# Kernel tuning notes

Hardware: AMD Instinct MI355X
Metric: run time of the kernel (lower is better)

Reference implementation:

```python
import jax, jax.numpy as jnp
from jax import lax
import numpy as np

V, E, H, F = 50257, 256, 512, 2
B, T = 128, 1024


def setup_inputs() -> dict:
    key = jax.random.key(0)
    ks = jax.random.split(key, 12)
    # zero-padded token ids: nonzero ids up to a random length, then 0-padding
    tok = jax.random.randint(ks[0], (B, T), 1, V)
    lengths = jax.random.randint(ks[1], (B,), 2, T + 1)  # at least 2 real tokens
    pos = jnp.arange(T)[None, :]
    tokens = jnp.where(pos < lengths[:, None], tok, 0)
    s = 0.02
    return {
        "tokens": tokens,
        "emb": jax.random.normal(ks[2], (V, E), jnp.float32) * s,
        "W_ih": jax.random.normal(ks[3], (4 * H, E), jnp.float32) * s,
        "b_ih": jax.random.normal(ks[4], (4 * H,), jnp.float32) * s,
        "W_hh": jax.random.normal(ks[5], (4 * H, H), jnp.float32) * s,
        "b_hh": jax.random.normal(ks[6], (4 * H,), jnp.float32) * s,
        "W_proj": jax.random.normal(ks[7], (H, 2 * H), jnp.float32) * s,
        "b_proj": jax.random.normal(ks[8], (H,), jnp.float32) * s,
        "W_out": jax.random.normal(ks[9], (F, H), jnp.float32) * s,
        "b_out": jax.random.normal(ks[10], (F,), jnp.float32) * s,
        "h0": jax.random.normal(ks[11], (B, H), jnp.float32),
        "c0": jax.random.normal(jax.random.fold_in(key, 99), (B, H), jnp.float32),
    }


def reference(tokens, emb, W_ih, b_ih, W_hh, b_hh, W_proj, b_proj, W_out, b_out, h0, c0):
    Bsz, Tlen = tokens.shape
    # sent_len = (index of first zero) - 1 ; if no zero, len(sent) - 1
    is_zero = tokens == 0
    first_zero = jnp.where(jnp.any(is_zero, axis=1), jnp.argmax(is_zero, axis=1), Tlen)
    sent_len = first_zero - 1  # negative wraps like python list indexing

    x = emb[tokens]  # [B, T, E]

    def step(carry, xt):
        h, c = carry
        gates = xt @ W_ih.T + b_ih + h @ W_hh.T + b_hh  # [B, 4H]
        i, f, g, o = jnp.split(gates, 4, axis=1)
        i = jax.nn.sigmoid(i)
        f = jax.nn.sigmoid(f)
        g = jnp.tanh(g)
        o = jax.nn.sigmoid(o)
        c = f * c + i * g
        h = o * jnp.tanh(c)
        return (h, c), (h, c)

    _, (hs, cs) = lax.scan(step, (h0, c0), jnp.swapaxes(x, 0, 1))  # [T, B, H]
    bidx = jnp.arange(Bsz)
    last = jnp.concatenate([hs[sent_len, bidx], cs[sent_len, bidx]], axis=1)  # [B, 2H]
    y = last @ W_proj.T + b_proj
    return y @ W_out.T + b_out
```

## Files before the change

### kernel.cpp

```cpp
#include <hip/hip_runtime.h>
#include <math.h>

#define B 128
#define T 1024
#define E 256
#define H 512

#define HBUF_OFF   0
#define LASTH_OFF  (2*65536)
#define LASTC_OFF  (3*65536)
#define FLAG_OFF   (4*65536)

__device__ __forceinline__ float sigm_f(float x) {
    return 1.f / (1.f + expf(-x));
}
__device__ __forceinline__ float tanh_f(float x) {
    return tanhf(x);
}

__device__ __forceinline__ void reduce32(float (&v)[32], int lane) {
#define RR(MASK, HALF)                                                 \
    {                                                                  \
        const bool hi = (lane & MASK) != 0;                            \
        _Pragma("unroll")                                              \
        for (int i = 0; i < HALF; ++i) {                               \
            const float mine   = hi ? v[i + HALF] : v[i];              \
            const float theirs = hi ? v[i] : v[i + HALF];              \
            v[i] = mine + __shfl_xor(theirs, MASK);                    \
        }                                                              \
    }
    RR(32, 16)
    RR(16, 8)
    RR(8, 4)
    RR(4, 2)
    RR(2, 1)
#undef RR
    v[0] = v[0] + __shfl_xor(v[0], 1);
}

__global__ __launch_bounds__(1024, 4) void lstm_persistent(
    const int* __restrict__ tokens, const float* __restrict__ emb,
    const float* __restrict__ W_ih, const float* __restrict__ b_ih,
    const float* __restrict__ W_hh, const float* __restrict__ b_hh,
    const float* __restrict__ h0, const float* __restrict__ c0,
    float* __restrict__ ws) {
    const int tid = threadIdx.x, bid = blockIdx.x;
    const int g = bid >> 5, m = bid & 31;

    float* h_buf  = ws + HBUF_OFF;
    float* last_h = ws + LASTH_OFF;
    float* last_c = ws + LASTC_OFF;
    int*   flags  = (int*)(ws + FLAG_OFF) + g * 64;

    __shared__ __align__(16) float xh[16 * 772];
    __shared__ float sgate[4][16][17];
    __shared__ int   s_L[16];
    __shared__ float s_c[256];
    __shared__ int   s_go;
    __shared__ float lds_pad[8192];

    {
        volatile float* vp = lds_pad;
        for (int i = tid; i < 8192; i += 1024) vp[i] = 0.f;
    }
    if (tid == 0) s_go = 0;

    if (tid < 16) s_L[tid] = T;
    __syncthreads();
    {
        const int b = tid >> 6;
        const int* tb = tokens + (size_t)(g * 16 + b) * T;
        int fz = T;
        for (int p = (tid & 63); p < T; p += 64)
            if (tb[p] == 0) fz = min(fz, p);
        atomicMin(&s_L[b], fz);
    }
    __syncthreads();
    if (tid < 16) {
        const int f = s_L[tid];
        s_L[tid] = (f == 0 || f == T) ? T : f;
    }
    __syncthreads();
    int Tg = 0;
#pragma unroll
    for (int i = 0; i < 16; ++i) Tg = max(Tg, s_L[i]);

    if (tid < 256) {
        const int uli = tid >> 4, bi = tid & 15;
        s_c[tid] = c0[(size_t)(g * 16 + bi) * H + (m * 16 + uli)];
    }

    {
        const int b = tid >> 6, kq4 = tid & 63;
        const int tok = tokens[(size_t)(g * 16 + b) * T + 0];
        ((float4*)&xh[b * 772])[kq4] =
            ((const float4*)emb)[(size_t)tok * 64 + kq4];
    }

    const int lane = tid & 63;
    const int w    = tid >> 6;
    const int unit = m * 16 + w;
    const float4* Wi4 = (const float4*)W_ih;
    const float4* Wh4 = (const float4*)W_hh;
    float4 wx[4], wh0[4], wh1[4];
#pragma unroll
    for (int G = 0; G < 4; ++G) {
        wx[G]  = Wi4[((size_t)G * H + unit) * 64 + lane];
        wh0[G] = Wh4[((size_t)G * H + unit) * 128 + lane];
        wh1[G] = Wh4[((size_t)G * H + unit) * 128 + 64 + lane];
    }

    const int ul2 = tid >> 4, b2 = tid & 15;
    const int unit2 = m * 16 + (ul2 & 15);
    const int bg = g * 16 + b2;
    const float bi_i = b_ih[unit2],         bh_i = b_hh[unit2];
    const float bi_f = b_ih[H + unit2],     bh_f = b_hh[H + unit2];
    const float bi_g = b_ih[2 * H + unit2], bh_g = b_hh[2 * H + unit2];
    const float bi_o = b_ih[3 * H + unit2], bh_o = b_hh[3 * H + unit2];

    __syncthreads();

    float v[32];

    for (int t = 0; t < Tg; ++t) {
#pragma unroll
        for (int bb = 0; bb < 8; ++bb) {
            const float4 x = ((const float4*)&xh[bb * 772])[lane];
#pragma unroll
            for (int G = 0; G < 4; ++G) {
                float p = wx[G].x * x.x;
                p = fmaf(wx[G].y, x.y, p);
                p = fmaf(wx[G].z, x.z, p);
                p = fmaf(wx[G].w, x.w, p);
                v[G * 8 + bb] = p;
            }
        }

        if (t > 0) {
            if (tid < 64) {
                const int* slot = &flags[tid & 31];
                while (true) {
                    const int fv = __hip_atomic_load(slot, __ATOMIC_RELAXED,
                                                     __HIP_MEMORY_SCOPE_AGENT);
                    if (__all(fv >= t)) break;
                    __builtin_amdgcn_s_sleep(1);
                }
                if (tid == 0)
                    __hip_atomic_store(&s_go, t, __ATOMIC_RELAXED,
                                       __HIP_MEMORY_SCOPE_WORKGROUP);
            } else {
                while (__hip_atomic_load(&s_go, __ATOMIC_RELAXED,
                                         __HIP_MEMORY_SCOPE_WORKGROUP) < t)
                    __builtin_amdgcn_s_sleep(1);
            }
        }

        if (t == 0) {
            const int b = tid >> 6, l = tid & 63;
            const float4* h04 = (const float4*)(h0 + (size_t)(g * 16 + b) * H);
            float4* dst = (float4*)&xh[b * 772 + 256];
            dst[l]      = h04[l];
            dst[64 + l] = h04[64 + l];
        } else {
            const unsigned long long* hs8 = (const unsigned long long*)
                (h_buf + (size_t)(t & 1) * (H * B));
            float2 hv[4];
#pragma unroll
            for (int j = 0; j < 4; ++j) {
                const int idx = j * 1024 + tid;
                const int u = idx >> 3, bp = idx & 7;
                unsigned long long val = __hip_atomic_load(
                    &hs8[(size_t)u * 64 + g * 8 + bp],
                    __ATOMIC_RELAXED, __HIP_MEMORY_SCOPE_AGENT);
                hv[j] = __builtin_bit_cast(float2, val);
            }
#pragma unroll
            for (int j = 0; j < 4; ++j) {
                const int idx = j * 1024 + tid;
                const int u = idx >> 3, bp = idx & 7;
                xh[(2 * bp) * 772 + 256 + u]     = hv[j].x;
                xh[(2 * bp + 1) * 772 + 256 + u] = hv[j].y;
            }
        }
        __syncthreads();

#pragma unroll
        for (int bb = 0; bb < 8; ++bb) {
            const float4 ha = ((const float4*)&xh[bb * 772])[64 + lane];
            const float4 hb = ((const float4*)&xh[bb * 772])[128 + lane];
#pragma unroll
            for (int G = 0; G < 4; ++G) {
                float p = v[G * 8 + bb];
                p = fmaf(wh0[G].x, ha.x, p);
                p = fmaf(wh0[G].y, ha.y, p);
                p = fmaf(wh0[G].z, ha.z, p);
                p = fmaf(wh0[G].w, ha.w, p);
                p = fmaf(wh1[G].x, hb.x, p);
                p = fmaf(wh1[G].y, hb.y, p);
                p = fmaf(wh1[G].z, hb.z, p);
                p = fmaf(wh1[G].w, hb.w, p);
                v[G * 8 + bb] = p;
            }
        }
        reduce32(v, lane);
        if ((lane & 1) == 0) {
            const int vi = (lane >> 1) & 31;
            sgate[vi >> 3][w][vi & 7] = v[0];
        }

#pragma unroll
        for (int bb = 0; bb < 8; ++bb) {
            const float4 x  = ((const float4*)&xh[(8 + bb) * 772])[lane];
            const float4 ha = ((const float4*)&xh[(8 + bb) * 772])[64 + lane];
            const float4 hb = ((const float4*)&xh[(8 + bb) * 772])[128 + lane];
#pragma unroll
            for (int G = 0; G < 4; ++G) {
                float p = wx[G].x * x.x;
                p = fmaf(wx[G].y, x.y, p);
                p = fmaf(wx[G].z, x.z, p);
                p = fmaf(wx[G].w, x.w, p);
                p = fmaf(wh0[G].x, ha.x, p);
                p = fmaf(wh0[G].y, ha.y, p);
                p = fmaf(wh0[G].z, ha.z, p);
                p = fmaf(wh0[G].w, ha.w, p);
                p = fmaf(wh1[G].x, hb.x, p);
                p = fmaf(wh1[G].y, hb.y, p);
                p = fmaf(wh1[G].z, hb.z, p);
                p = fmaf(wh1[G].w, hb.w, p);
                v[G * 8 + bb] = p;
            }
        }
        reduce32(v, lane);
        if ((lane & 1) == 0) {
            const int vi = (lane >> 1) & 31;
            sgate[vi >> 3][w][8 + (vi & 7)] = v[0];
        }

        float4 xreg;
        const bool do_stage = (t + 1 < Tg);
        if (do_stage) {
            const int b = tid >> 6, kq4 = tid & 63;
            const int tok = tokens[(size_t)(g * 16 + b) * T + (t + 1)];
            xreg = ((const float4*)emb)[(size_t)tok * 64 + kq4];
        }
        __syncthreads();

        if (tid < 256) {
            const float ai = sgate[0][ul2][b2] + bi_i + bh_i;
            const float af = sgate[1][ul2][b2] + bi_f + bh_f;
            const float ag = sgate[2][ul2][b2] + bi_g + bh_g;
            const float ao = sgate[3][ul2][b2] + bi_o + bh_o;

            const float ig = sigm_f(ai);
            const float fg = sigm_f(af);
            const float gv = tanh_f(ag);
            const float og = sigm_f(ao);

            const float c_old = s_c[tid];
            const float c_new = fg * c_old + ig * gv;
            const float h_new = og * tanh_f(c_new);
            s_c[tid] = c_new;

            const int idx = unit2 * B + bg;
            __hip_atomic_store(&h_buf[(size_t)((t + 1) & 1) * (H * B) + idx],
                               h_new, __ATOMIC_RELAXED,
                               __HIP_MEMORY_SCOPE_AGENT);
            if (t == s_L[b2] - 1) {
                last_h[idx] = h_new;
                last_c[idx] = c_new;
            }
        }

        if (do_stage) {
            __syncthreads();
            if (tid == 0)
                __hip_atomic_store(&flags[m], t + 1, __ATOMIC_RELAXED,
                                   __HIP_MEMORY_SCOPE_AGENT);
            {
                const int b = tid >> 6, kq4 = tid & 63;
                ((float4*)&xh[b * 772])[kq4] = xreg;
            }
            __syncthreads();
        }
    }
}

__global__ __launch_bounds__(256) void final_kernel(
    const float* __restrict__ ws_ro, const float* __restrict__ W_proj,
    const float* __restrict__ b_proj, const float* __restrict__ W_out,
    const float* __restrict__ b_out, float* __restrict__ out) {
    const int bg = blockIdx.x, tid = threadIdx.x;
    const float* last_h = ws_ro + LASTH_OFF;
    const float* last_c = ws_ro + LASTC_OFF;

    __shared__ __align__(16) float s_hc[2 * H];
    __shared__ float s_y[H];
    for (int u = tid; u < H; u += 256) {
        s_hc[u]     = last_h[u * B + bg];
        s_hc[H + u] = last_c[u * B + bg];
    }
    __syncthreads();

    const float4* hc4 = (const float4*)s_hc;
    const float4* Wp4 = (const float4*)W_proj;
#pragma unroll
    for (int jj = 0; jj < 2; ++jj) {
        const int j = tid + jj * 256;
        const float4* wr = Wp4 + (size_t)j * 256;
        float4 acc = {0, 0, 0, 0};
#pragma unroll 4
        for (int kq = 0; kq < 256; ++kq) {
            acc.x = fmaf(wr[kq].x, hc4[kq].x, acc.x);
            acc.y = fmaf(wr[kq].y, hc4[kq].y, acc.y);
            acc.z = fmaf(wr[kq].z, hc4[kq].z, acc.z);
            acc.w = fmaf(wr[kq].w, hc4[kq].w, acc.w);
        }
        s_y[j] = acc.x + acc.y + acc.z + acc.w + b_proj[j];
    }
    __syncthreads();

    if (tid < 64) {
        float p0 = 0.f, p1 = 0.f;
        for (int j = tid; j < H; j += 64) {
            const float y = s_y[j];
            p0 = fmaf(y, W_out[j], p0);
            p1 = fmaf(y, W_out[H + j], p1);
        }
#pragma unroll
        for (int off = 32; off; off >>= 1) {
            p0 += __shfl_down(p0, off);
            p1 += __shfl_down(p1, off);
        }
        if (tid == 0) {
            out[bg * 2 + 0] = p0 + b_out[0];
            out[bg * 2 + 1] = p1 + b_out[1];
        }
    }
}

extern "C" void kernel_launch(void* const* d_in, const int* in_sizes, int n_in,
                              void* d_out, int out_size, void* d_ws, size_t ws_size,
                              hipStream_t stream) {
    const int*   tokens = (const int*)d_in[0];
    const float* emb    = (const float*)d_in[1];
    const float* W_ih   = (const float*)d_in[2];
    const float* b_ih   = (const float*)d_in[3];
    const float* W_hh   = (const float*)d_in[4];
    const float* b_hh   = (const float*)d_in[5];
    const float* W_proj = (const float*)d_in[6];
    const float* b_proj = (const float*)d_in[7];
    const float* W_out  = (const float*)d_in[8];
    const float* b_out  = (const float*)d_in[9];
    const float* h0     = (const float*)d_in[10];
    const float* c0     = (const float*)d_in[11];
    float* out = (float*)d_out;
    float* ws  = (float*)d_ws;

    hipMemsetAsync((char*)d_ws + (size_t)FLAG_OFF * sizeof(float), 0,
                   8 * 64 * sizeof(int), stream);

    void* kargs[] = {(void*)&tokens, (void*)&emb, (void*)&W_ih, (void*)&b_ih,
                     (void*)&W_hh, (void*)&b_hh, (void*)&h0, (void*)&c0,
                     (void*)&ws};
    hipLaunchCooperativeKernel((const void*)lstm_persistent, dim3(256),
                               dim3(1024), kargs, 0, stream);

    hipLaunchKernelGGL(final_kernel, dim3(B), dim3(256), 0, stream,
                       ws, W_proj, b_proj, W_out, b_out, out);
}
```

Baseline: 8.781 ms.

## Halve LSTM block size, compute two hidden units per wave, drop a barrier

The persistent LSTM kernel now runs 512-thread blocks. Each wave keeps the W_ih/W_hh rows for two hidden units in registers and computes both units' gate dot products, so the register tiling per thread doubles. Token embedding and h0 staging loops are rewritten for the smaller block. The next-step embedding is now written into shared memory before the remaining barrier, which removes one __syncthreads per timestep. The aim is to cut per-step barrier cost and improve reuse of the x/h values loaded from shared memory, at the cost of more registers per thread and fewer waves to hide latency on the serial recurrence.

Measured after the change: 11.19 ms. 27.5% more time.

```diff
diff --git a/kernel.cpp b/kernel.cpp
--- a/kernel.cpp
+++ b/kernel.cpp
@@ -38,7 +38,7 @@
     v[0] = v[0] + __shfl_xor(v[0], 1);
 }
 
-__global__ __launch_bounds__(1024, 4) void lstm_persistent(
+__global__ __launch_bounds__(512, 2) void lstm_persistent(
     const int* __restrict__ tokens, const float* __restrict__ emb,
     const float* __restrict__ W_ih, const float* __restrict__ b_ih,
     const float* __restrict__ W_hh, const float* __restrict__ b_hh,
@@ -61,17 +61,17 @@
 
     {
         volatile float* vp = lds_pad;
-        for (int i = tid; i < 8192; i += 1024) vp[i] = 0.f;
+        for (int i = tid; i < 8192; i += 512) vp[i] = 0.f;
     }
     if (tid == 0) s_go = 0;
 
     if (tid < 16) s_L[tid] = T;
     __syncthreads();
     {
-        const int b = tid >> 6;
+        const int b = tid >> 5;
         const int* tb = tokens + (size_t)(g * 16 + b) * T;
         int fz = T;
-        for (int p = (tid & 63); p < T; p += 64)
+        for (int p = (tid & 31); p < T; p += 32)
             if (tb[p] == 0) fz = min(fz, p);
         atomicMin(&s_L[b], fz);
     }
@@ -91,23 +91,30 @@
     }
 
     {
-        const int b = tid >> 6, kq4 = tid & 63;
+        const int b = tid >> 5, j = tid & 31;
         const int tok = tokens[(size_t)(g * 16 + b) * T + 0];
-        ((float4*)&xh[b * 772])[kq4] =
-            ((const float4*)emb)[(size_t)tok * 64 + kq4];
+        const float4* er = ((const float4*)emb) + (size_t)tok * 64;
+        float4* dst = (float4*)&xh[b * 772];
+        dst[j]      = er[j];
+        dst[32 + j] = er[32 + j];
     }
 
     const int lane = tid & 63;
     const int w    = tid >> 6;
-    const int unit = m * 16 + w;
+    const int uA   = m * 16 + 2 * w;
+    const int uB   = uA + 1;
     const float4* Wi4 = (const float4*)W_ih;
     const float4* Wh4 = (const float4*)W_hh;
-    float4 wx[4], wh0[4], wh1[4];
+    float4 wxA[4], whA0[4], whA1[4];
+    float4 wxB[4], whB0[4], whB1[4];
 #pragma unroll
     for (int G = 0; G < 4; ++G) {
-        wx[G]  = Wi4[((size_t)G * H + unit) * 64 + lane];
-        wh0[G] = Wh4[((size_t)G * H + unit) * 128 + lane];
-        wh1[G] = Wh4[((size_t)G * H + unit) * 128 + 64 + lane];
+        wxA[G]  = Wi4[((size_t)G * H + uA) * 64 + lane];
+        whA0[G] = Wh4[((size_t)G * H + uA) * 128 + lane];
+        whA1[G] = Wh4[((size_t)G * H + uA) * 128 + 64 + lane];
+        wxB[G]  = Wi4[((size_t)G * H + uB) * 64 + lane];
+        whB0[G] = Wh4[((size_t)G * H + uB) * 128 + lane];
+        whB1[G] = Wh4[((size_t)G * H + uB) * 128 + 64 + lane];
     }
 
     const int ul2 = tid >> 4, b2 = tid & 15;
@@ -120,7 +127,7 @@
 
     __syncthreads();
 
-    float v[32];
+    float vA[32], vB[32];
 
     for (int t = 0; t < Tg; ++t) {
 #pragma unroll
@@ -128,11 +135,16 @@
             const float4 x = ((const float4*)&xh[bb * 772])[lane];
 #pragma unroll
             for (int G = 0; G < 4; ++G) {
-                float p = wx[G].x * x.x;
-                p = fmaf(wx[G].y, x.y, p);
-                p = fmaf(wx[G].z, x.z, p);
-                p = fmaf(wx[G].w, x.w, p);
-                v[G * 8 + bb] = p;
+                float p = wxA[G].x * x.x;
+                p = fmaf(wxA[G].y, x.y, p);
+                p = fmaf(wxA[G].z, x.z, p);
+                p = fmaf(wxA[G].w, x.w, p);
+                vA[G * 8 + bb] = p;
+                float q = wxB[G].x * x.x;
+                q = fmaf(wxB[G].y, x.y, q);
+                q = fmaf(wxB[G].z, x.z, q);
+                q = fmaf(wxB[G].w, x.w, q);
+                vB[G * 8 + bb] = q;
             }
         }
 
@@ -156,18 +168,20 @@
         }
 
         if (t == 0) {
-            const int b = tid >> 6, l = tid & 63;
+            const int b = tid >> 5, l = tid & 31;
             const float4* h04 = (const float4*)(h0 + (size_t)(g * 16 + b) * H);
             float4* dst = (float4*)&xh[b * 772 + 256];
             dst[l]      = h04[l];
+            dst[32 + l] = h04[32 + l];
             dst[64 + l] = h04[64 + l];
+            dst[96 + l] = h04[96 + l];
         } else {
             const unsigned long long* hs8 = (const unsigned long long*)
                 (h_buf + (size_t)(t & 1) * (H * B));
-            float2 hv[4];
-#pragma unroll
-            for (int j = 0; j < 4; ++j) {
-                const int idx = j * 1024 + tid;
+            float2 hv[8];
+#pragma unroll
+            for (int j = 0; j < 8; ++j) {
+                const int idx = j * 512 + tid;
                 const int u = idx >> 3, bp = idx & 7;
                 unsigned long long val = __hip_atomic_load(
                     &hs8[(size_t)u * 64 + g * 8 + bp],
@@ -175,8 +189,8 @@
                 hv[j] = __builtin_bit_cast(float2, val);
             }
 #pragma unroll
-            for (int j = 0; j < 4; ++j) {
-                const int idx = j * 1024 + tid;
+            for (int j = 0; j < 8; ++j) {
+                const int idx = j * 512 + tid;
                 const int u = idx >> 3, bp = idx & 7;
                 xh[(2 * bp) * 772 + 256 + u]     = hv[j].x;
                 xh[(2 * bp + 1) * 772 + 256 + u] = hv[j].y;
@@ -190,22 +204,37 @@
             const float4 hb = ((const float4*)&xh[bb * 772])[128 + lane];
 #pragma unroll
             for (int G = 0; G < 4; ++G) {
-                float p = v[G * 8 + bb];
-                p = fmaf(wh0[G].x, ha.x, p);
-                p = fmaf(wh0[G].y, ha.y, p);
-                p = fmaf(wh0[G].z, ha.z, p);
-                p = fmaf(wh0[G].w, ha.w, p);
-                p = fmaf(wh1[G].x, hb.x, p);
-                p = fmaf(wh1[G].y, hb.y, p);
-                p = fmaf(wh1[G].z, hb.z, p);
-                p = fmaf(wh1[G].w, hb.w, p);
-                v[G * 8 + bb] = p;
-            }
-        }
-        reduce32(v, lane);
+                float p = vA[G * 8 + bb];
+                p = fmaf(whA0[G].x, ha.x, p);
+                p = fmaf(whA0[G].y, ha.y, p);
+                p = fmaf(whA0[G].z, ha.z, p);
+                p = fmaf(whA0[G].w, ha.w, p);
+                p = fmaf(whA1[G].x, hb.x, p);
+                p = fmaf(whA1[G].y, hb.y, p);
+                p = fmaf(whA1[G].z, hb.z, p);
+                p = fmaf(whA1[G].w, hb.w, p);
+                vA[G * 8 + bb] = p;
+                float q = vB[G * 8 + bb];
+                q = fmaf(whB0[G].x, ha.x, q);
+                q = fmaf(whB0[G].y, ha.y, q);
+                q = fmaf(whB0[G].z, ha.z, q);
+                q = fmaf(whB0[G].w, ha.w, q);
+                q = fmaf(whB1[G].x, hb.x, q);
+                q = fmaf(whB1[G].y, hb.y, q);
+                q = fmaf(whB1[G].z, hb.z, q);
+                q = fmaf(whB1[G].w, hb.w, q);
+                vB[G * 8 + bb] = q;
+            }
+        }
+        reduce32(vA, lane);
         if ((lane & 1) == 0) {
             const int vi = (lane >> 1) & 31;
-            sgate[vi >> 3][w][vi & 7] = v[0];
+            sgate[vi >> 3][2 * w][vi & 7] = vA[0];
+        }
+        reduce32(vB, lane);
+        if ((lane & 1) == 0) {
+            const int vi = (lane >> 1) & 31;
+            sgate[vi >> 3][2 * w + 1][vi & 7] = vB[0];
         }
 
 #pragma unroll
@@ -215,33 +244,53 @@
             const float4 hb = ((const float4*)&xh[(8 + bb) * 772])[128 + lane];
 #pragma unroll
             for (int G = 0; G < 4; ++G) {
-                float p = wx[G].x * x.x;
-                p = fmaf(wx[G].y, x.y, p);
-                p = fmaf(wx[G].z, x.z, p);
-                p = fmaf(wx[G].w, x.w, p);
-                p = fmaf(wh0[G].x, ha.x, p);
-                p = fmaf(wh0[G].y, ha.y, p);
-                p = fmaf(wh0[G].z, ha.z, p);
-                p = fmaf(wh0[G].w, ha.w, p);
-                p = fmaf(wh1[G].x, hb.x, p);
-                p = fmaf(wh1[G].y, hb.y, p);
-                p = fmaf(wh1[G].z, hb.z, p);
-                p = fmaf(wh1[G].w, hb.w, p);
-                v[G * 8 + bb] = p;
-            }
-        }
-        reduce32(v, lane);
+                float p = wxA[G].x * x.x;
+                p = fmaf(wxA[G].y, x.y, p);
+                p = fmaf(wxA[G].z, x.z, p);
+                p = fmaf(wxA[G].w, x.w, p);
+                p = fmaf(whA0[G].x, ha.x, p);
+                p = fmaf(whA0[G].y, ha.y, p);
+                p = fmaf(whA0[G].z, ha.z, p);
+                p = fmaf(whA0[G].w, ha.w, p);
+                p = fmaf(whA1[G].x, hb.x, p);
+                p = fmaf(whA1[G].y, hb.y, p);
+                p = fmaf(whA1[G].z, hb.z, p);
+                p = fmaf(whA1[G].w, hb.w, p);
+                vA[G * 8 + bb] = p;
+                float q = wxB[G].x * x.x;
+                q = fmaf(wxB[G].y, x.y, q);
+                q = fmaf(wxB[G].z, x.z, q);
+                q = fmaf(wxB[G].w, x.w, q);
+                q = fmaf(whB0[G].x, ha.x, q);
+                q = fmaf(whB0[G].y, ha.y, q);
+                q = fmaf(whB0[G].z, ha.z, q);
+                q = fmaf(whB0[G].w, ha.w, q);
+                q = fmaf(whB1[G].x, hb.x, q);
+                q = fmaf(whB1[G].y, hb.y, q);
+                q = fmaf(whB1[G].z, hb.z, q);
+                q = fmaf(whB1[G].w, hb.w, q);
+                vB[G * 8 + bb] = q;
+            }
+        }
+        reduce32(vA, lane);
         if ((lane & 1) == 0) {
             const int vi = (lane >> 1) & 31;
-            sgate[vi >> 3][w][8 + (vi & 7)] = v[0];
-        }
-
-        float4 xreg;
+            sgate[vi >> 3][2 * w][8 + (vi & 7)] = vA[0];
+        }
+        reduce32(vB, lane);
+        if ((lane & 1) == 0) {
+            const int vi = (lane >> 1) & 31;
+            sgate[vi >> 3][2 * w + 1][8 + (vi & 7)] = vB[0];
+        }
+
+        float4 xregA, xregB;
         const bool do_stage = (t + 1 < Tg);
         if (do_stage) {
-            const int b = tid >> 6, kq4 = tid & 63;
+            const int b = tid >> 5, j = tid & 31;
             const int tok = tokens[(size_t)(g * 16 + b) * T + (t + 1)];
-            xreg = ((const float4*)emb)[(size_t)tok * 64 + kq4];
+            const float4* er = ((const float4*)emb) + (size_t)tok * 64;
+            xregA = er[j];
+            xregB = er[32 + j];
         }
         __syncthreads();
 
@@ -270,17 +319,16 @@
                 last_c[idx] = c_new;
             }
         }
-
         if (do_stage) {
+            const int b = tid >> 5, j = tid & 31;
+            float4* dst = (float4*)&xh[b * 772];
+            dst[j]      = xregA;
+            dst[32 + j] = xregB;
+
             __syncthreads();
             if (tid == 0)
                 __hip_atomic_store(&flags[m], t + 1, __ATOMIC_RELAXED,
                                    __HIP_MEMORY_SCOPE_AGENT);
-            {
-                const int b = tid >> 6, kq4 = tid & 63;
-                ((float4*)&xh[b * 772])[kq4] = xreg;
-            }
-            __syncthreads();
         }
     }
 }
@@ -363,7 +411,7 @@
                      (void*)&W_hh, (void*)&b_hh, (void*)&h0, (void*)&c0,
                      (void*)&ws};
     hipLaunchCooperativeKernel((const void*)lstm_persistent, dim3(256),
-                               dim3(1024), kargs, 0, stream);
+                               dim3(512), kargs, 0, stream);
 
     hipLaunchKernelGGL(final_kernel, dim3(B), dim3(256), 0, stream,
                        ws, W_proj, b_proj, W_out, b_out, out);
```
